# Optimization experiments

Hardware: AMD Instinct MI355X
Metric: run time of the kernel (lower is better)

The kernel has to match this reference:

```python
import jax, jax.numpy as jnp
import numpy as np

B, X, C = 8, 256, 256  # batch, feature axis, topfreq

def setup_inputs() -> dict:
    key = jax.random.key(0)
    k1, k2, k3, k4 = jax.random.split(key, 4)
    return {
        "amplitude": jax.random.normal(k1, (B, X, C), dtype=jnp.float32),
        "phase": jax.random.normal(k2, (B, X, C), dtype=jnp.float32),
        "A": jax.random.normal(k3, (C, C), dtype=jnp.float32),
        "w_amplitude": jnp.asarray(0.5, dtype=jnp.float32),
        "w_phase": jnp.asarray(0.5, dtype=jnp.float32),
        # uniform noise for gumbel sampling; keep away from 0 to avoid -log(-log(0))
        "gumbel_u": jax.random.uniform(k4, (B, C, C, 2), dtype=jnp.float32, minval=1e-6, maxval=1.0),
    }

def reference(amplitude, phase, A, w_amplitude, w_phase, gumbel_u):
    # pairwise diffs: (b, x, c, c)
    a_diff = amplitude[..., :, None] - amplitude[..., None, :]
    p_diff = phase[..., :, None] - phase[..., None, :]
    fused = w_amplitude * a_diff + w_phase * p_diff
    # einsum 'dd,bxcd->bxcd' == multiply by diag(A) along last dim
    temp = jnp.diagonal(A) * fused
    # einsum 'bxcd,bxcd->bcd' == sum of squares over x
    dist = jnp.sum(temp * temp, axis=1)  # (b, c, c)
    exp_dist = 1.0 / (dist + 1e-10)
    eye = jnp.eye(C, dtype=exp_dist.dtype)
    off_diag = 1.0 - eye
    exp_dist = exp_dist * off_diag
    exp_max = jax.lax.stop_gradient(jnp.max(exp_dist, axis=-1, keepdims=True))
    p = exp_dist / exp_max
    p = (p * off_diag + eye) * 0.99  # (b, c, c) in (0, 0.99]
    # bernoulli via 2-class gumbel-softmax (tau=1, hard, straight-through)
    logit = jnp.log(p / (1.0 - p))
    logits = jnp.stack([logit, -logit], axis=-1)  # (b, c, c, 2)
    g = -jnp.log(-jnp.log(gumbel_u))
    y = jax.nn.softmax(logits + g, axis=-1)
    y0 = y[..., 0]
    hard0 = (y0 > y[..., 1]).astype(y.dtype)
    sample = hard0 - jax.lax.stop_gradient(y0) + y0  # straight-through
    mask = sample.mean(axis=0)  # (c, c)
    return mask
```

## Files before the change

### kernel.cpp

```cpp
#include <hip/hip_runtime.h>

#define BB 8
#define XX 256
#define CC 256
#define TCD 8
#define TCE 4
#define G  8
#define SPLIT 4
#define XH (XX / SPLIT)



__global__ __launch_bounds__(256) void k_u(
    const float* __restrict__ amp, const float* __restrict__ ph,
    const float* __restrict__ wAp, const float* __restrict__ wPp,
    float* __restrict__ u, float* __restrict__ out)
{
    const float wa = wAp[0], wp = wPp[0];
    const int i = blockIdx.x * 256 + threadIdx.x;
    const float4 a = ((const float4*)amp)[i];
    const float4 p = ((const float4*)ph)[i];
    float4 r;
    r.x = __fadd_rn(__fmul_rn(wa, a.x), __fmul_rn(wp, p.x));
    r.y = __fadd_rn(__fmul_rn(wa, a.y), __fmul_rn(wp, p.y));
    r.z = __fadd_rn(__fmul_rn(wa, a.z), __fmul_rn(wp, p.z));
    r.w = __fadd_rn(__fmul_rn(wa, a.w), __fmul_rn(wp, p.w));
    ((float4*)u)[i] = r;

    if (blockIdx.x < 64) {
        ((float4*)out)[blockIdx.x * 256 + threadIdx.x] = make_float4(0.f, 0.f, 0.f, 0.f);
    }
}

#define ULOAD(BU, GIDX) {                                  \
    const float* _p = ud_ptr + (size_t)(GIDX) * G * CC;    \
    _Pragma("unroll")                                      \
    for (int i = 0; i < G; ++i) BU[i] = _p[(size_t)i * CC]; }

#define UCOMP(BU, GIDX) {                                  \
    const int _xb = (GIDX) * G;                            \
    _Pragma("unroll")                                      \
    for (int i = 0; i < G; ++i) {                          \
        const float udv = BU[i];                           \
        const float4 cA = *(const float4*)(ucol + (size_t)(_xb + i) * CC);     \
        const float4 cB = *(const float4*)(ucol + (size_t)(_xb + i) * CC + 4); \
        gacc0 = fmaf(cA.x, udv, gacc0);                    \
        gacc1 = fmaf(cA.y, udv, gacc1);                    \
        gacc2 = fmaf(cA.z, udv, gacc2);                    \
        gacc3 = fmaf(cA.w, udv, gacc3);                    \
        gacc4 = fmaf(cB.x, udv, gacc4);                    \
        gacc5 = fmaf(cB.y, udv, gacc5);                    \
        gacc6 = fmaf(cB.z, udv, gacc6);                    \
        gacc7 = fmaf(cB.w, udv, gacc7);                    \
        sacc  = fmaf(udv, udv, sacc);                      \
    } }

__global__ __launch_bounds__(256, 4) void k_dist(
    const float* __restrict__ u,
    float* __restrict__ wsd)
{
    const int d    = threadIdx.x;
    const int c0   = blockIdx.x * TCD;
    const int b    = blockIdx.y;
    const int x0   = blockIdx.z * XH;

    const float* ucol = u + ((size_t)b * XX + x0) * CC + c0;
    const float* ud_ptr = u + ((size_t)b * XX + x0) * CC + d;

    float gacc0 = 0.f, gacc1 = 0.f, gacc2 = 0.f, gacc3 = 0.f;
    float gacc4 = 0.f, gacc5 = 0.f, gacc6 = 0.f, gacc7 = 0.f, sacc = 0.f;

    constexpr int NGH = XH / G;
    float b0[G], b1[G];
    ULOAD(b0, 0)
    for (int g = 0; g + 2 < NGH; g += 2) {
        ULOAD(b1, g + 1)
        UCOMP(b0, g)
        ULOAD(b0, g + 2)
        UCOMP(b1, g + 1)
    }
    ULOAD(b1, NGH - 1)
    UCOMP(b0, NGH - 2)
    UCOMP(b1, NGH - 1)

    __shared__ float sS[CC];
    sS[d] = sacc;
    __syncthreads();

    float* w = wsd + (((size_t)blockIdx.z * BB + b) * CC + c0) * CC + d;
    w[0 * CC] = fmaf(-2.0f, gacc0, __fadd_rn(sS[c0 + 0], sacc));
    w[1 * CC] = fmaf(-2.0f, gacc1, __fadd_rn(sS[c0 + 1], sacc));
    w[2 * CC] = fmaf(-2.0f, gacc2, __fadd_rn(sS[c0 + 2], sacc));
    w[3 * CC] = fmaf(-2.0f, gacc3, __fadd_rn(sS[c0 + 3], sacc));
    w[4 * CC] = fmaf(-2.0f, gacc4, __fadd_rn(sS[c0 + 4], sacc));
    w[5 * CC] = fmaf(-2.0f, gacc5, __fadd_rn(sS[c0 + 5], sacc));
    w[6 * CC] = fmaf(-2.0f, gacc6, __fadd_rn(sS[c0 + 6], sacc));
    w[7 * CC] = fmaf(-2.0f, gacc7, __fadd_rn(sS[c0 + 7], sacc));
}

__global__ __launch_bounds__(256, 4) void k_epi(
    const float* __restrict__ wsd, const float* __restrict__ A,
    const float* __restrict__ gu,  float* __restrict__ out)
{
    const int d  = threadIdx.x;
    const int c0 = blockIdx.x * TCE;
    const int b  = blockIdx.y;

    const float dAd  = A[(size_t)d * CC + d];
    const float dAd2 = __fmul_rn(dAd, dAd);

    float dist[TCE];
#pragma unroll
    for (int j = 0; j < TCE; ++j) {
        const size_t ro = ((size_t)b * CC + c0 + j) * CC + d;
        float p = wsd[ro];
#pragma unroll
        for (int h = 1; h < SPLIT; ++h)
            p = __fadd_rn(p, wsd[(size_t)h * BB * CC * CC + ro]);
        dist[j] = __fmul_rn(dAd2, p);
    }

    float ed[TCE];
#pragma unroll
    for (int j = 0; j < TCE; ++j)
        ed[j] = (d == c0 + j) ? 0.0f : __fdiv_rn(1.0f, __fadd_rn(dist[j], 1e-10f));

    __shared__ float wmax[TCE][4];
    const int wave = threadIdx.x >> 6;
    const int lane = threadIdx.x & 63;
#pragma unroll
    for (int j = 0; j < TCE; ++j) {
        float v = ed[j];
#pragma unroll
        for (int m = 1; m < 64; m <<= 1) v = fmaxf(v, __shfl_xor(v, m));
        if (lane == 0) wmax[j][wave] = v;
    }
    __syncthreads();

#pragma unroll
    for (int j = 0; j < TCE; ++j) {
        const int c = c0 + j;
        float em = fmaxf(fmaxf(wmax[j][0], wmax[j][1]), fmaxf(wmax[j][2], wmax[j][3]));
        float p;
        if (d == c) {
            p = 0.99f;
        } else {
            p = __fmul_rn(__fdiv_rn(ed[j], em), 0.99f);
        }
        float logit = logf(__fdiv_rn(p, __fsub_rn(1.0f, p)));

        const float2 g2 = *(const float2*)(gu + (((size_t)b * CC + c) * CC + d) * 2);
        float g0 = -logf(-logf(g2.x));
        float g1 = -logf(-logf(g2.y));

        float a0 = __fadd_rn(logit, g0);
        float a1 = __fadd_rn(-logit, g1);
        float m  = fmaxf(a0, a1);
        float e0 = expf(__fsub_rn(a0, m));
        float e1 = expf(__fsub_rn(a1, m));
        float s  = __fadd_rn(e0, e1);
        float y0 = __fdiv_rn(e0, s);
        float y1 = __fdiv_rn(e1, s);
        if (y0 > y1) {
            atomicAdd(&out[(size_t)c * CC + d], 0.125f);
        }
    }
}


#define STEPU(UC, ACC) {                         \
    float diff = __fsub_rn(UC, ud);              \
    float t    = __fmul_rn(dAd, diff);           \
    float sq   = __fmul_rn(t, t);                \
    ACC = __fadd_rn(ACC, sq);                    \
}

#define LOADG(BA, BP, GIDX) {                    \
    const float* _a = ampbd + (size_t)(GIDX) * G * CC; \
    const float* _p = phbd  + (size_t)(GIDX) * G * CC; \
    _Pragma("unroll")                            \
    for (int i = 0; i < G; ++i) {                \
        BA[i] = _a[(size_t)i * CC];              \
        BP[i] = _p[(size_t)i * CC];              \
    }                                            \
}

#define COMPG(BA, BP, GIDX) {                    \
    const int _xb = (GIDX) * G;                  \
    _Pragma("unroll")                            \
    for (int i = 0; i < G; ++i) {                \
        const float av = BA[i];                  \
        const float pv = BP[i];                  \
        const float ud = __fadd_rn(__fmul_rn(wa, av), __fmul_rn(wp, pv)); \
        const float4 uc = cols[_xb + i];         \
        STEPU(uc.x, acc0)                        \
        STEPU(uc.y, acc1)                        \
        STEPU(uc.z, acc2)                        \
        STEPU(uc.w, acc3)                        \
    }                                            \
}

__global__ __launch_bounds__(256, 2) void k_fused(
    const float* __restrict__ amp, const float* __restrict__ ph,
    const float* __restrict__ A,   const float* __restrict__ wAp,
    const float* __restrict__ wPp, const float* __restrict__ gu,
    float* __restrict__ out)
{
    const int d  = threadIdx.x;
    const int c0 = blockIdx.x * TCE;
    const int b  = blockIdx.y;

    const float wa = wAp[0];
    const float wp = wPp[0];

    __shared__ float4 cols[XX];
    {
        const int x = threadIdx.x;
        const size_t base = ((size_t)b * XX + x) * CC + c0;
        const float4 a4 = *(const float4*)(amp + base);
        const float4 p4 = *(const float4*)(ph  + base);
        float4 uu;
        uu.x = __fadd_rn(__fmul_rn(wa, a4.x), __fmul_rn(wp, p4.x));
        uu.y = __fadd_rn(__fmul_rn(wa, a4.y), __fmul_rn(wp, p4.y));
        uu.z = __fadd_rn(__fmul_rn(wa, a4.z), __fmul_rn(wp, p4.z));
        uu.w = __fadd_rn(__fmul_rn(wa, a4.w), __fmul_rn(wp, p4.w));
        cols[x] = uu;
    }
    __syncthreads();

    const float dAd = A[(size_t)d * CC + d];
    const float* ampbd = amp + (size_t)b * XX * CC + d;
    const float* phbd  = ph  + (size_t)b * XX * CC + d;

    float acc0 = 0.0f, acc1 = 0.0f, acc2 = 0.0f, acc3 = 0.0f;
    constexpr int NG = XX / G;
    {
        float b0A[G], b0P[G], b1A[G], b1P[G];
        LOADG(b0A, b0P, 0)
        for (int g = 0; g + 2 < NG; g += 2) {
            LOADG(b1A, b1P, g + 1)
            COMPG(b0A, b0P, g)
            LOADG(b0A, b0P, g + 2)
            COMPG(b1A, b1P, g + 1)
        }
        LOADG(b1A, b1P, NG - 1)
        COMPG(b0A, b0P, NG - 2)
        COMPG(b1A, b1P, NG - 1)
    }

    float ed[TCE];
    ed[0] = (d == c0)     ? 0.0f : __fdiv_rn(1.0f, __fadd_rn(acc0, 1e-10f));
    ed[1] = (d == c0 + 1) ? 0.0f : __fdiv_rn(1.0f, __fadd_rn(acc1, 1e-10f));
    ed[2] = (d == c0 + 2) ? 0.0f : __fdiv_rn(1.0f, __fadd_rn(acc2, 1e-10f));
    ed[3] = (d == c0 + 3) ? 0.0f : __fdiv_rn(1.0f, __fadd_rn(acc3, 1e-10f));

    __shared__ float wmax[TCE][4];
    const int wave = threadIdx.x >> 6;
    const int lane = threadIdx.x & 63;
#pragma unroll
    for (int j = 0; j < TCE; ++j) {
        float v = ed[j];
#pragma unroll
        for (int m = 1; m < 64; m <<= 1) v = fmaxf(v, __shfl_xor(v, m));
        if (lane == 0) wmax[j][wave] = v;
    }
    __syncthreads();

#pragma unroll
    for (int j = 0; j < TCE; ++j) {
        const int c = c0 + j;
        float em = fmaxf(fmaxf(wmax[j][0], wmax[j][1]), fmaxf(wmax[j][2], wmax[j][3]));
        float p;
        if (d == c) {
            p = 0.99f;
        } else {
            p = __fmul_rn(__fdiv_rn(ed[j], em), 0.99f);
        }
        float logit = logf(__fdiv_rn(p, __fsub_rn(1.0f, p)));

        const float2 g2 = *(const float2*)(gu + (((size_t)b * CC + c) * CC + d) * 2);
        float g0 = -logf(-logf(g2.x));
        float g1 = -logf(-logf(g2.y));

        float a0 = __fadd_rn(logit, g0);
        float a1 = __fadd_rn(-logit, g1);
        float m  = fmaxf(a0, a1);
        float e0 = expf(__fsub_rn(a0, m));
        float e1 = expf(__fsub_rn(a1, m));
        float s  = __fadd_rn(e0, e1);
        float y0 = __fdiv_rn(e0, s);
        float y1 = __fdiv_rn(e1, s);
        if (y0 > y1) {
            atomicAdd(&out[(size_t)c * CC + d], 0.125f);
        }
    }
}

extern "C" void kernel_launch(void* const* d_in, const int* in_sizes, int n_in,
                              void* d_out, int out_size, void* d_ws, size_t ws_size,
                              hipStream_t stream) {
    const float* amp = (const float*)d_in[0];
    const float* ph  = (const float*)d_in[1];
    const float* A   = (const float*)d_in[2];
    const float* wa  = (const float*)d_in[3];
    const float* wp  = (const float*)d_in[4];
    const float* gu  = (const float*)d_in[5];
    float* out = (float*)d_out;

    const size_t uElems = (size_t)BB * XX * CC;
    const size_t pElems = (size_t)SPLIT * BB * CC * CC;
    const size_t need = (uElems + pElems) * sizeof(float);
    if (ws_size >= need) {
        float* ud  = (float*)d_ws;
        float* wsd = ud + uElems;
        k_u<<<uElems / 4 / 256, 256, 0, stream>>>(amp, ph, wa, wp, ud, out);
        dim3 g1(CC / TCD, BB, SPLIT);
        k_dist<<<g1, 256, 0, stream>>>(ud, wsd);
        dim3 g2(CC / TCE, BB);
        k_epi<<<g2, 256, 0, stream>>>(wsd, A, gu, out);
    } else {
        hipMemsetAsync(out, 0, (size_t)CC * CC * sizeof(float), stream);
        dim3 g(CC / TCE, BB);
        k_fused<<<g, 256, 0, stream>>>(amp, ph, A, wa, wp, gu, out);
    }
}
```

Baseline: 84.44 us.

## Restructure k_dist into per-wave x-slices with shared column tile and float4 d-tiles

Each wave in k_dist now handles its own 16-row x slice, raising the split count to 16. Each thread computes a 4-wide d tile (float4 loads) against 8 columns staged once in shared memory, in a fully unrolled pipeline. The aim is more register reuse per loaded value and vectorized loads and stores. In exchange, the partial-sum workspace quadruples, so k_epi must read and sum 16 partials per element; it now issues all those loads up front for memory-level parallelism.

```diff
diff --git a/kernel.cpp b/kernel.cpp
--- a/kernel.cpp
+++ b/kernel.cpp
@@ -5,9 +5,10 @@
 #define CC 256
 #define TCD 8
 #define TCE 4
-#define G  8
-#define SPLIT 4
+#define TD 4
+#define SPLIT 16
 #define XH (XX / SPLIT)
+#define GX 4
 
 
 
@@ -32,70 +33,93 @@
     }
 }
 
-#define ULOAD(BU, GIDX) {                                  \
-    const float* _p = ud_ptr + (size_t)(GIDX) * G * CC;    \
-    _Pragma("unroll")                                      \
-    for (int i = 0; i < G; ++i) BU[i] = _p[(size_t)i * CC]; }
-
-#define UCOMP(BU, GIDX) {                                  \
-    const int _xb = (GIDX) * G;                            \
-    _Pragma("unroll")                                      \
-    for (int i = 0; i < G; ++i) {                          \
-        const float udv = BU[i];                           \
-        const float4 cA = *(const float4*)(ucol + (size_t)(_xb + i) * CC);     \
-        const float4 cB = *(const float4*)(ucol + (size_t)(_xb + i) * CC + 4); \
-        gacc0 = fmaf(cA.x, udv, gacc0);                    \
-        gacc1 = fmaf(cA.y, udv, gacc1);                    \
-        gacc2 = fmaf(cA.z, udv, gacc2);                    \
-        gacc3 = fmaf(cA.w, udv, gacc3);                    \
-        gacc4 = fmaf(cB.x, udv, gacc4);                    \
-        gacc5 = fmaf(cB.y, udv, gacc5);                    \
-        gacc6 = fmaf(cB.z, udv, gacc6);                    \
-        gacc7 = fmaf(cB.w, udv, gacc7);                    \
-        sacc  = fmaf(udv, udv, sacc);                      \
+#define ULOAD4(BU, GIDX) {                                        \
+    const float* _p = ud_base + (size_t)(GIDX) * GX * CC;         \
+    _Pragma("unroll")                                             \
+    for (int i = 0; i < GX; ++i)                                  \
+        BU[i] = *(const float4*)(_p + (size_t)i * CC);            }
+
+#define UCOMP4(BU, GIDX) {                                        \
+    const int _xb = xloc + (GIDX) * GX;                           \
+    _Pragma("unroll")                                             \
+    for (int i = 0; i < GX; ++i) {                                \
+        const float4 ud4 = BU[i];                                 \
+        const float4 cA = cols[_xb + i][0];                       \
+        const float4 cB = cols[_xb + i][1];                       \
+        _Pragma("unroll")                                         \
+        for (int k = 0; k < 4; ++k) {                             \
+            const float uv = (k==0)?ud4.x:(k==1)?ud4.y:(k==2)?ud4.z:ud4.w; \
+            gacc[0][k] = fmaf(cA.x, uv, gacc[0][k]);              \
+            gacc[1][k] = fmaf(cA.y, uv, gacc[1][k]);              \
+            gacc[2][k] = fmaf(cA.z, uv, gacc[2][k]);              \
+            gacc[3][k] = fmaf(cA.w, uv, gacc[3][k]);              \
+            gacc[4][k] = fmaf(cB.x, uv, gacc[4][k]);              \
+            gacc[5][k] = fmaf(cB.y, uv, gacc[5][k]);              \
+            gacc[6][k] = fmaf(cB.z, uv, gacc[6][k]);              \
+            gacc[7][k] = fmaf(cB.w, uv, gacc[7][k]);              \
+            sacc[k]    = fmaf(uv, uv, sacc[k]);                   \
+        }                                                         \
     } }
 
 __global__ __launch_bounds__(256, 4) void k_dist(
     const float* __restrict__ u,
     float* __restrict__ wsd)
 {
-    const int d    = threadIdx.x;
+    const int tid  = threadIdx.x;
+    const int lane = tid & 63;
+    const int w    = tid >> 6;
     const int c0   = blockIdx.x * TCD;
     const int b    = blockIdx.y;
-    const int x0   = blockIdx.z * XH;
-
-    const float* ucol = u + ((size_t)b * XX + x0) * CC + c0;
-    const float* ud_ptr = u + ((size_t)b * XX + x0) * CC + d;
-
-    float gacc0 = 0.f, gacc1 = 0.f, gacc2 = 0.f, gacc3 = 0.f;
-    float gacc4 = 0.f, gacc5 = 0.f, gacc6 = 0.f, gacc7 = 0.f, sacc = 0.f;
-
-    constexpr int NGH = XH / G;
-    float b0[G], b1[G];
-    ULOAD(b0, 0)
-    for (int g = 0; g + 2 < NGH; g += 2) {
-        ULOAD(b1, g + 1)
-        UCOMP(b0, g)
-        ULOAD(b0, g + 2)
-        UCOMP(b1, g + 1)
-    }
-    ULOAD(b1, NGH - 1)
-    UCOMP(b0, NGH - 2)
-    UCOMP(b1, NGH - 1)
-
-    __shared__ float sS[CC];
-    sS[d] = sacc;
-    __syncthreads();
-
-    float* w = wsd + (((size_t)blockIdx.z * BB + b) * CC + c0) * CC + d;
-    w[0 * CC] = fmaf(-2.0f, gacc0, __fadd_rn(sS[c0 + 0], sacc));
-    w[1 * CC] = fmaf(-2.0f, gacc1, __fadd_rn(sS[c0 + 1], sacc));
-    w[2 * CC] = fmaf(-2.0f, gacc2, __fadd_rn(sS[c0 + 2], sacc));
-    w[3 * CC] = fmaf(-2.0f, gacc3, __fadd_rn(sS[c0 + 3], sacc));
-    w[4 * CC] = fmaf(-2.0f, gacc4, __fadd_rn(sS[c0 + 4], sacc));
-    w[5 * CC] = fmaf(-2.0f, gacc5, __fadd_rn(sS[c0 + 5], sacc));
-    w[6 * CC] = fmaf(-2.0f, gacc6, __fadd_rn(sS[c0 + 6], sacc));
-    w[7 * CC] = fmaf(-2.0f, gacc7, __fadd_rn(sS[c0 + 7], sacc));
+    const int cz   = blockIdx.z * 4 + w;
+    const int x0b  = blockIdx.z * 64;
+    const int xloc = w * XH;
+    const int d0   = lane * TD;
+
+    __shared__ float4 cols[64][2];
+    if (tid < 128) {
+        const int x = tid >> 1, h = tid & 1;
+        cols[x][h] = *(const float4*)(u + ((size_t)b * XX + x0b + x) * CC + c0 + 4 * h);
+    }
+    __syncthreads();
+
+    const float* ud_base = u + ((size_t)b * XX + x0b + xloc) * CC + d0;
+
+    float gacc[TCD][4];
+#pragma unroll
+    for (int j = 0; j < TCD; ++j)
+#pragma unroll
+        for (int k = 0; k < 4; ++k) gacc[j][k] = 0.0f;
+    float sacc[4] = {0.f, 0.f, 0.f, 0.f};
+
+    constexpr int NG = XH / GX;
+    {
+        float4 b0[GX], b1[GX];
+        ULOAD4(b0, 0)
+        ULOAD4(b1, 1)
+        UCOMP4(b0, 0)
+        ULOAD4(b0, 2)
+        UCOMP4(b1, 1)
+        ULOAD4(b1, 3)
+        UCOMP4(b0, 2)
+        UCOMP4(b1, 3)
+        static_assert(NG == 4, "pipeline hard-coded for NG==4");
+    }
+
+    __shared__ float sS[4][CC];
+    *(float4*)&sS[w][d0] = make_float4(sacc[0], sacc[1], sacc[2], sacc[3]);
+    __syncthreads();
+
+    float* wbase = wsd + (((size_t)cz * BB + b) * CC + c0) * CC + d0;
+#pragma unroll
+    for (int j = 0; j < TCD; ++j) {
+        const float scj = sS[w][c0 + j];
+        float4 o;
+        o.x = fmaf(-2.0f, gacc[j][0], __fadd_rn(scj, sacc[0]));
+        o.y = fmaf(-2.0f, gacc[j][1], __fadd_rn(scj, sacc[1]));
+        o.z = fmaf(-2.0f, gacc[j][2], __fadd_rn(scj, sacc[2]));
+        o.w = fmaf(-2.0f, gacc[j][3], __fadd_rn(scj, sacc[3]));
+        *(float4*)(wbase + (size_t)j * CC) = o;
+    }
 }
 
 __global__ __launch_bounds__(256, 4) void k_epi(
@@ -109,14 +133,21 @@
     const float dAd  = A[(size_t)d * CC + d];
     const float dAd2 = __fmul_rn(dAd, dAd);
 
+    float pv[TCE][SPLIT];
+#pragma unroll
+    for (int j = 0; j < TCE; ++j) {
+        const size_t ro = ((size_t)b * CC + c0 + j) * CC + d;
+#pragma unroll
+        for (int h = 0; h < SPLIT; ++h)
+            pv[j][h] = wsd[(size_t)h * BB * CC * CC + ro];
+    }
+
     float dist[TCE];
 #pragma unroll
     for (int j = 0; j < TCE; ++j) {
-        const size_t ro = ((size_t)b * CC + c0 + j) * CC + d;
-        float p = wsd[ro];
-#pragma unroll
-        for (int h = 1; h < SPLIT; ++h)
-            p = __fadd_rn(p, wsd[(size_t)h * BB * CC * CC + ro]);
+        float p = pv[j][0];
+#pragma unroll
+        for (int h = 1; h < SPLIT; ++h) p = __fadd_rn(p, pv[j][h]);
         dist[j] = __fmul_rn(dAd2, p);
     }
 
@@ -176,19 +207,19 @@
 }
 
 #define LOADG(BA, BP, GIDX) {                    \
-    const float* _a = ampbd + (size_t)(GIDX) * G * CC; \
-    const float* _p = phbd  + (size_t)(GIDX) * G * CC; \
+    const float* _a = ampbd + (size_t)(GIDX) * 8 * CC; \
+    const float* _p = phbd  + (size_t)(GIDX) * 8 * CC; \
     _Pragma("unroll")                            \
-    for (int i = 0; i < G; ++i) {                \
+    for (int i = 0; i < 8; ++i) {                \
         BA[i] = _a[(size_t)i * CC];              \
         BP[i] = _p[(size_t)i * CC];              \
     }                                            \
 }
 
 #define COMPG(BA, BP, GIDX) {                    \
-    const int _xb = (GIDX) * G;                  \
+    const int _xb = (GIDX) * 8;                  \
     _Pragma("unroll")                            \
-    for (int i = 0; i < G; ++i) {                \
+    for (int i = 0; i < 8; ++i) {                \
         const float av = BA[i];                  \
         const float pv = BP[i];                  \
         const float ud = __fadd_rn(__fmul_rn(wa, av), __fmul_rn(wp, pv)); \
@@ -233,9 +264,9 @@
     const float* phbd  = ph  + (size_t)b * XX * CC + d;
 
     float acc0 = 0.0f, acc1 = 0.0f, acc2 = 0.0f, acc3 = 0.0f;
-    constexpr int NG = XX / G;
+    constexpr int NG = XX / 8;
     {
-        float b0A[G], b0P[G], b1A[G], b1P[G];
+        float b0A[8], b0P[8], b1A[8], b1P[8];
         LOADG(b0A, b0P, 0)
         for (int g = 0; g + 2 < NG; g += 2) {
             LOADG(b1A, b1P, g + 1)
@@ -314,7 +345,7 @@
         float* ud  = (float*)d_ws;
         float* wsd = ud + uElems;
         k_u<<<uElems / 4 / 256, 256, 0, stream>>>(amp, ph, wa, wp, ud, out);
-        dim3 g1(CC / TCD, BB, SPLIT);
+        dim3 g1(CC / TCD, BB, SPLIT / 4);
         k_dist<<<g1, 256, 0, stream>>>(ud, wsd);
         dim3 g2(CC / TCE, BB);
         k_epi<<<g2, 256, 0, stream>>>(wsd, A, gu, out);
```

Result: slower. 93.83 us (+11.1%).
